# Optimization experiments

Measured on AMD Instinct MI355X. Metric: run time of the kernel, lower is better.

## Reference

```python
import jax, jax.numpy as jnp
import numpy as np

N = 8192
IN_F = 512
OUT_F = 128
NUM_CLASSES = 10
ALPHA = 0.2  # LeakyReLU negative slope
NEG_INF = -9e15


def setup_inputs() -> dict:
    key = jax.random.key(0)
    k_h, k_d, k_W, k_a, k_cw, k_cb = jax.random.split(key, 6)
    h = jax.random.normal(k_h, (N, IN_F), dtype=jnp.float32)
    dist = jax.random.randint(k_d, (N, N), 0, 2, dtype=jnp.int32)
    # xavier_uniform with gain=1.414
    gain = 1.414
    lim_W = gain * np.sqrt(6.0 / (IN_F + OUT_F))
    W = jax.random.uniform(k_W, (IN_F, OUT_F), minval=-lim_W, maxval=lim_W, dtype=jnp.float32)
    lim_a = gain * np.sqrt(6.0 / (2 * OUT_F + 1))
    a = jax.random.uniform(k_a, (2 * OUT_F, 1), minval=-lim_a, maxval=lim_a, dtype=jnp.float32)
    # nn.Linear(out_features, num_classes): weight [C, out], bias [C]
    lim_c = np.sqrt(1.0 / OUT_F)
    Wc = jax.random.uniform(k_cw, (NUM_CLASSES, OUT_F), minval=-lim_c, maxval=lim_c, dtype=jnp.float32)
    bc = jax.random.uniform(k_cb, (NUM_CLASSES,), minval=-lim_c, maxval=lim_c, dtype=jnp.float32)
    return {"h": h, "dist": dist, "W": W, "a": a, "Wc": Wc, "bc": bc}


def reference(h, dist, W, a, Wc, bc):
    Wh = h @ W                              # [N, out]
    Wh1 = Wh @ a[:OUT_F]                    # [N, 1]
    Wh2 = Wh @ a[OUT_F:]                    # [N, 1]
    e = jax.nn.leaky_relu(Wh1 + Wh2.T, negative_slope=ALPHA)  # [N, N]
    att = jnp.where(dist > 0, e, NEG_INF)
    att = jax.nn.softmax(att, axis=1)       # [N, N]
    h_update = jax.nn.elu(att @ Wh)         # [N, out] (dropout inactive at inference)
    y_pred = h_update @ Wc.T + bc           # [N, num_classes]
    return y_pred
```

## Files before the change

### kernel.cpp

```cpp
#include <hip/hip_runtime.h>
#include <stdint.h>

#define N 8192
#define IN_F 512
#define OUT_F 128
#define NCLS 10
#define ALPHA 0.2f

typedef float f32x4 __attribute__((ext_vector_type(4)));
typedef int   i32x4 __attribute__((ext_vector_type(4)));
typedef short s16x4 __attribute__((ext_vector_type(4)));
typedef short s16x8 __attribute__((ext_vector_type(8)));

__device__ __forceinline__ short f2bf(float x) {
    unsigned u = __builtin_bit_cast(unsigned, x);
    u = (u + 0x7FFFu + ((u >> 16) & 1u)) >> 16;
    return (short)u;
}
__device__ __forceinline__ float bf2f(short s) {
    unsigned u = ((unsigned)(unsigned short)s) << 16;
    return __builtin_bit_cast(float, u);
}

__global__ void split_w_kernel(const float* __restrict__ W,
                               short* __restrict__ WThi, short* __restrict__ WTlo) {
    int idx = blockIdx.x * 256 + threadIdx.x;
    int k = idx >> 7, col = idx & 127;
    float x = W[idx];
    short hi = f2bf(x);
    short lo = f2bf(x - bf2f(hi));
    size_t a = (size_t)(k >> 5) * (128 * 32) + (size_t)col * 32 + (k & 31);
    WThi[a] = hi;
    WTlo[a] = lo;
}

#define WH_ROWS 16
#define WH_STR 520

__global__ __launch_bounds__(256, 2)
void wh_kernel(const float* __restrict__ h, const short* __restrict__ WThi,
               const short* __restrict__ WTlo, const float* __restrict__ a,
               short* __restrict__ WhT, float* __restrict__ Wh1,
               float* __restrict__ Wh2) {
    __shared__ __align__(16) short Ahi[WH_ROWS][WH_STR];
    __shared__ __align__(16) short Alo[WH_ROWS][WH_STR];
    __shared__ __align__(16) float whs[WH_ROWS][OUT_F + 4];

    const int t = threadIdx.x;
    const int r0 = blockIdx.x * WH_ROWS;

    {
        int row = t >> 4, c4 = t & 15;
        const float* hrow = h + (size_t)(r0 + row) * IN_F;
        #pragma unroll
        for (int jj = 0; jj < 4; ++jj) {
            int k0 = c4 * 8 + jj * 128;
            f32x4 x0 = *(const f32x4*)(hrow + k0);
            f32x4 x1 = *(const f32x4*)(hrow + k0 + 4);
            s16x8 hi, lo;
            #pragma unroll
            for (int e = 0; e < 4; ++e) {
                short h0 = f2bf(x0[e]); hi[e] = h0; lo[e] = f2bf(x0[e] - bf2f(h0));
                short h1 = f2bf(x1[e]); hi[4 + e] = h1; lo[4 + e] = f2bf(x1[e] - bf2f(h1));
            }
            *(s16x8*)&Ahi[row][k0] = hi;
            *(s16x8*)&Alo[row][k0] = lo;
        }
    }
    __syncthreads();

    const int lane = t & 63, w = t >> 6;
    const int q = lane >> 4, ln16 = lane & 15;
    f32x4 acc[2] = {};
    #pragma unroll
    for (int kc = 0; kc < IN_F / 32; ++kc) {
        s16x8 ahi = *(const s16x8*)&Ahi[ln16][kc * 32 + q * 8];
        s16x8 alo = *(const s16x8*)&Alo[ln16][kc * 32 + q * 8];
        #pragma unroll
        for (int nt = 0; nt < 2; ++nt) {
            int col = w * 32 + nt * 16 + ln16;
            size_t boff = (size_t)kc * 4096 + (size_t)col * 32 + q * 8;
            s16x8 bhi = *(const s16x8*)(WThi + boff);
            s16x8 blo = *(const s16x8*)(WTlo + boff);
            acc[nt] = __builtin_amdgcn_mfma_f32_16x16x32_bf16(ahi, bhi, acc[nt], 0, 0, 0);
            acc[nt] = __builtin_amdgcn_mfma_f32_16x16x32_bf16(ahi, blo, acc[nt], 0, 0, 0);
            acc[nt] = __builtin_amdgcn_mfma_f32_16x16x32_bf16(alo, bhi, acc[nt], 0, 0, 0);
        }
    }
    #pragma unroll
    for (int nt = 0; nt < 2; ++nt)
        #pragma unroll
        for (int reg = 0; reg < 4; ++reg)
            whs[q * 4 + reg][w * 32 + nt * 16 + ln16] = acc[nt][reg];
    __syncthreads();

    if (t < 128) {
        int r = t >> 3, s = t & 7;
        float s1 = 0.f, s2 = 0.f;
        #pragma unroll
        for (int cc = 0; cc < 16; ++cc) {
            int c = s * 16 + cc;
            float v = whs[r][c];
            s1 = fmaf(v, a[c], s1);
            s2 = fmaf(v, a[OUT_F + c], s2);
        }
        s1 += __shfl_xor(s1, 1); s1 += __shfl_xor(s1, 2); s1 += __shfl_xor(s1, 4);
        s2 += __shfl_xor(s2, 1); s2 += __shfl_xor(s2, 2); s2 += __shfl_xor(s2, 4);
        if (s == 0) { Wh1[r0 + r] = s1; Wh2[r0 + r] = s2; }
    }

    {
        int c = t >> 1, h8 = t & 1;
        s16x8 pack;
        #pragma unroll
        for (int rr = 0; rr < 8; ++rr) pack[rr] = f2bf(whs[h8 * 8 + rr][c]);
        size_t addr = (size_t)(r0 >> 5) * 4096 + (size_t)c * 32 + (r0 & 16) + h8 * 8;
        *(s16x8*)(WhT + addr) = pack;
    }
}

#define BK 128

__global__ __launch_bounds__(256, 4)
void attn_kernel(const int* __restrict__ dist, const short* __restrict__ WhT,
                 const float* __restrict__ Wh1v, const float* __restrict__ Wh2v,
                 float* __restrict__ acc_part, float* __restrict__ l_part,
                 int nit) {
    const int t = threadIdx.x;
    const int it = blockIdx.x & 127;
    const int sp = blockIdx.x >> 7;
    const int i0 = it * 64;
    const int lane = t & 63, w = t >> 6;
    const int q = lane >> 4, m = lane & 15;
    const int row = i0 + w * 16 + m;
    const int j0 = sp * nit * BK;

    const int* __restrict__ drow = dist + (size_t)row * N + j0;
    const float* __restrict__ wh2p = Wh2v + j0;
    const float wh1 = Wh1v[row];
    float l_acc = 0.f;
    f32x4 acc[8] = {};

    for (int kt = 0; kt < nit; ++kt) {
        const int jb = kt * BK;
        i32x4 d[8];
        #pragma unroll
        for (int kc = 0; kc < 4; ++kc) {
            d[kc * 2]     = *(const i32x4*)(drow + jb + kc * 32 + q * 8);
            d[kc * 2 + 1] = *(const i32x4*)(drow + jb + kc * 32 + q * 8 + 4);
        }
        s16x8 afr[4];
        #pragma unroll
        for (int kc = 0; kc < 4; ++kc) {
            const float* w2p = wh2p + jb + kc * 32 + q * 8;
            f32x4 w20 = *(const f32x4*)(w2p);
            f32x4 w21 = *(const f32x4*)(w2p + 4);
            #pragma unroll
            for (int e = 0; e < 4; ++e) {
                float sv = wh1 + w20[e];
                float lr = fmaxf(sv, ALPHA * sv);
                float pv = (d[kc * 2][e] > 0) ? __expf(lr) : 0.f;
                l_acc += pv;
                unsigned u = __builtin_bit_cast(unsigned, pv);
                afr[kc][e] = (short)((u + 0x8000u) >> 16);
                float sv1 = wh1 + w21[e];
                float lr1 = fmaxf(sv1, ALPHA * sv1);
                float pv1 = (d[kc * 2 + 1][e] > 0) ? __expf(lr1) : 0.f;
                l_acc += pv1;
                unsigned u1 = __builtin_bit_cast(unsigned, pv1);
                afr[kc][4 + e] = (short)((u1 + 0x8000u) >> 16);
            }
        }
        const short* bb = WhT + (size_t)((j0 + jb) >> 5) * 4096 + q * 8;
        #pragma unroll
        for (int kc = 0; kc < 4; ++kc) {
            const short* bkc = bb + (size_t)kc * 4096;
            #pragma unroll
            for (int nt = 0; nt < 8; ++nt) {
                s16x8 bfr = *(const s16x8*)(bkc + (nt * 16 + m) * 32);
                acc[nt] = __builtin_amdgcn_mfma_f32_16x16x32_bf16(afr[kc], bfr, acc[nt], 0, 0, 0);
            }
        }
    }

    l_acc += __shfl_xor(l_acc, 16);
    l_acc += __shfl_xor(l_acc, 32);
    if (q == 0) l_part[(size_t)sp * N + row] = l_acc;

    float* ap = acc_part + (size_t)sp * N * OUT_F
              + ((size_t)i0 + w * 16 + q * 4) * OUT_F + m;
    #pragma unroll
    for (int reg = 0; reg < 4; ++reg)
        #pragma unroll
        for (int nt = 0; nt < 8; ++nt)
            ap[(size_t)reg * OUT_F + nt * 16] = acc[nt][reg];
}

__global__ __launch_bounds__(256, 4)
void reduce_kernel(const float* __restrict__ acc_part, const float* __restrict__ l_part,
                   const float* __restrict__ Wc, const float* __restrict__ bcv,
                   float* __restrict__ out, int split) {
    __shared__ __align__(16) float hu[16][OUT_F + 4];
    const int t = threadIdx.x;
    const int i0 = blockIdx.x * 16;
    const int row = t >> 4, cg = t & 15;

    f32x4 v0 = {0.f, 0.f, 0.f, 0.f}, v1 = {0.f, 0.f, 0.f, 0.f};
    float l = 0.f;
    for (int s = 0; s < split; ++s) {
        const float* ap = acc_part + (size_t)s * N * OUT_F + (size_t)(i0 + row) * OUT_F + cg * 8;
        v0 += *(const f32x4*)ap;
        v1 += *(const f32x4*)(ap + 4);
        l += l_part[(size_t)s * N + i0 + row];
    }
    float inv = 1.f / l;
    #pragma unroll
    for (int e = 0; e < 4; ++e) {
        float x0 = v0[e] * inv; x0 = x0 > 0.f ? x0 : (__expf(x0) - 1.f);
        float x1 = v1[e] * inv; x1 = x1 > 0.f ? x1 : (__expf(x1) - 1.f);
        hu[row][cg * 8 + e] = x0;
        hu[row][cg * 8 + 4 + e] = x1;
    }
    __syncthreads();

    if (t < 16 * NCLS) {
        int rr = t / NCLS, cls = t - rr * NCLS;
        const f32x4* hurow = (const f32x4*)&hu[rr][0];
        const f32x4* wcrow = (const f32x4*)(Wc + cls * OUT_F);
        float sum = bcv[cls];
        #pragma unroll 8
        for (int c4 = 0; c4 < OUT_F / 4; ++c4) {
            f32x4 hv = hurow[c4];
            f32x4 wv = wcrow[c4];
            sum += hv[0] * wv[0] + hv[1] * wv[1] + hv[2] * wv[2] + hv[3] * wv[3];
        }
        out[(size_t)(i0 + rr) * NCLS + cls] = sum;
    }
}

extern "C" void kernel_launch(void* const* d_in, const int* in_sizes, int n_in,
                              void* d_out, int out_size, void* d_ws, size_t ws_size,
                              hipStream_t stream) {
    const float* h    = (const float*)d_in[0];
    const int*   dist = (const int*)d_in[1];
    const float* W    = (const float*)d_in[2];
    const float* a    = (const float*)d_in[3];
    const float* Wc   = (const float*)d_in[4];
    const float* bc   = (const float*)d_in[5];
    float* out = (float*)d_out;

    char* ws = (char*)d_ws;
    size_t off = 0;
    short* WhT  = (short*)(ws + off); off += (size_t)OUT_F * N * 2;
    short* WThi = (short*)(ws + off); off += (size_t)IN_F * OUT_F * 2;
    short* WTlo = (short*)(ws + off); off += (size_t)IN_F * OUT_F * 2;
    float* Wh1  = (float*)(ws + off); off += (size_t)N * 4;
    float* Wh2  = (float*)(ws + off); off += (size_t)N * 4;

    size_t per_split = (size_t)N * OUT_F * 4 + (size_t)N * 4;
    int split = 8;
    while (split > 1 && off + (size_t)split * per_split > ws_size) split >>= 1;
    float* acc_part = (float*)(ws + off); off += (size_t)split * N * OUT_F * 4;
    float* l_part   = (float*)(ws + off);

    hipLaunchKernelGGL(split_w_kernel, dim3(256), dim3(256), 0, stream, W, WThi, WTlo);
    hipLaunchKernelGGL(wh_kernel, dim3(N / WH_ROWS), dim3(256), 0, stream,
                       h, WThi, WTlo, a, WhT, Wh1, Wh2);
    int nit = N / (BK * split);
    hipLaunchKernelGGL(attn_kernel, dim3(128 * split), dim3(256), 0, stream,
                       dist, WhT, Wh1, Wh2, acc_part, l_part, nit);
    hipLaunchKernelGGL(reduce_kernel, dim3(N / 16), dim3(256), 0, stream,
                       acc_part, l_part, Wc, bc, out, split);
}
```

Measured before the change: 501.6 us.

## Prefetch next dist tile in registers and stagger tile order per block

```diff
diff --git a/kernel.cpp b/kernel.cpp
--- a/kernel.cpp
+++ b/kernel.cpp
@@ -134,6 +134,7 @@
     const int q = lane >> 4, m = lane & 15;
     const int row = i0 + w * 16 + m;
     const int j0 = sp * nit * BK;
+    const int phase = it & (nit - 1);
 
     const int* __restrict__ drow = dist + (size_t)row * N + j0;
     const float* __restrict__ wh2p = Wh2v + j0;
@@ -141,20 +142,50 @@
     float l_acc = 0.f;
     f32x4 acc[8] = {};
 
-    for (int kt = 0; kt < nit; ++kt) {
-        const int jb = kt * BK;
-        i32x4 d[8];
+    i32x4 d[8];
+    f32x4 w2[2][2];
+    {
+        const int jb = phase * BK;
         #pragma unroll
         for (int kc = 0; kc < 4; ++kc) {
             d[kc * 2]     = *(const i32x4*)(drow + jb + kc * 32 + q * 8);
             d[kc * 2 + 1] = *(const i32x4*)(drow + jb + kc * 32 + q * 8 + 4);
         }
+        w2[0][0] = *(const f32x4*)(wh2p + jb + 0 * 32 + q * 8);
+        w2[0][1] = *(const f32x4*)(wh2p + jb + 0 * 32 + q * 8 + 4);
+        w2[1][0] = *(const f32x4*)(wh2p + jb + 1 * 32 + q * 8);
+        w2[1][1] = *(const f32x4*)(wh2p + jb + 1 * 32 + q * 8 + 4);
+    }
+
+    for (int kt = 0; kt < nit; ++kt) {
+        const int cur = (kt + phase) & (nit - 1);
+        const int jb = cur * BK;
+        const bool more = (kt + 1) < nit;
+        const int jbn = (((kt + 1 + phase) & (nit - 1))) * BK;
+
+        i32x4 dn[8];
+        f32x4 w2n[2][2];
+        if (more) {
+            #pragma unroll
+            for (int kc = 0; kc < 4; ++kc) {
+                dn[kc * 2]     = *(const i32x4*)(drow + jbn + kc * 32 + q * 8);
+                dn[kc * 2 + 1] = *(const i32x4*)(drow + jbn + kc * 32 + q * 8 + 4);
+            }
+            w2n[0][0] = *(const f32x4*)(wh2p + jbn + 0 * 32 + q * 8);
+            w2n[0][1] = *(const f32x4*)(wh2p + jbn + 0 * 32 + q * 8 + 4);
+            w2n[1][0] = *(const f32x4*)(wh2p + jbn + 1 * 32 + q * 8);
+            w2n[1][1] = *(const f32x4*)(wh2p + jbn + 1 * 32 + q * 8 + 4);
+        }
+
         s16x8 afr[4];
         #pragma unroll
         for (int kc = 0; kc < 4; ++kc) {
-            const float* w2p = wh2p + jb + kc * 32 + q * 8;
-            f32x4 w20 = *(const f32x4*)(w2p);
-            f32x4 w21 = *(const f32x4*)(w2p + 4);
+            f32x4 w20, w21;
+            if (kc < 2) { w20 = w2[kc][0]; w21 = w2[kc][1]; }
+            else {
+                w20 = *(const f32x4*)(wh2p + jb + kc * 32 + q * 8);
+                w21 = *(const f32x4*)(wh2p + jb + kc * 32 + q * 8 + 4);
+            }
             #pragma unroll
             for (int e = 0; e < 4; ++e) {
                 float sv = wh1 + w20[e];
@@ -181,6 +212,12 @@
                 acc[nt] = __builtin_amdgcn_mfma_f32_16x16x32_bf16(afr[kc], bfr, acc[nt], 0, 0, 0);
             }
         }
+        if (more) {
+            #pragma unroll
+            for (int u = 0; u < 8; ++u) d[u] = dn[u];
+            #pragma unroll
+            for (int u = 0; u < 2; ++u) { w2[u][0] = w2n[u][0]; w2[u][1] = w2n[u][1]; }
+        }
     }
 
     l_acc += __shfl_xor(l_acc, 16);
```

Result: slower. 644.4 us (+28.5%).

## Prefetch dist tile into LDS bitmask with coalesced loads before MFMA loop

Applied to the files above, without the earlier changes.

```diff
diff --git a/kernel.cpp b/kernel.cpp
--- a/kernel.cpp
+++ b/kernel.cpp
@@ -7,9 +7,14 @@
 #define NCLS 10
 #define ALPHA 0.2f
 
+#define WCOLS 1024
+#define NSP (N / WCOLS)
+#define BK 128
+#define NIT (WCOLS / BK)
+#define MSTR 33
+
 typedef float f32x4 __attribute__((ext_vector_type(4)));
 typedef int   i32x4 __attribute__((ext_vector_type(4)));
-typedef short s16x4 __attribute__((ext_vector_type(4)));
 typedef short s16x8 __attribute__((ext_vector_type(8)));
 
 __device__ __forceinline__ short f2bf(float x) {
@@ -119,56 +124,70 @@
     }
 }
 
-#define BK 128
-
 __global__ __launch_bounds__(256, 4)
 void attn_kernel(const int* __restrict__ dist, const short* __restrict__ WhT,
                  const float* __restrict__ Wh1v, const float* __restrict__ Wh2v,
-                 float* __restrict__ acc_part, float* __restrict__ l_part,
-                 int nit) {
+                 float* __restrict__ acc_part, float* __restrict__ l_part) {
+    __shared__ unsigned maskL[64 * MSTR];
+    __shared__ __align__(16) float wh2L[WCOLS];
+
     const int t = threadIdx.x;
     const int it = blockIdx.x & 127;
     const int sp = blockIdx.x >> 7;
     const int i0 = it * 64;
+    const int j0 = sp * WCOLS;
     const int lane = t & 63, w = t >> 6;
     const int q = lane >> 4, m = lane & 15;
+
+    {
+        const int l = lane;
+        #pragma unroll 4
+        for (int rr = 0; rr < 16; ++rr) {
+            const int r = w * 16 + rr;
+            const int* rp = dist + (size_t)(i0 + r) * N + j0 + l * 4;
+            #pragma unroll
+            for (int p = 0; p < 4; ++p) {
+                i32x4 v = *(const i32x4*)(rp + p * 256);
+                unsigned nib = (unsigned)(v[0] > 0) | ((unsigned)(v[1] > 0) << 1)
+                             | ((unsigned)(v[2] > 0) << 2) | ((unsigned)(v[3] > 0) << 3);
+                unsigned b = nib | (__shfl_xor(nib, 1) << 4);
+                b = b | (__shfl_xor(b, 2) << 8);
+                b = b | (__shfl_xor(b, 4) << 16);
+                if ((l & 7) == 0) maskL[r * MSTR + p * 8 + (l >> 3)] = b;
+            }
+        }
+        if (t < WCOLS / 4)
+            *(f32x4*)&wh2L[t * 4] = *(const f32x4*)(Wh2v + j0 + t * 4);
+    }
+    __syncthreads();
+
     const int row = i0 + w * 16 + m;
-    const int j0 = sp * nit * BK;
-
-    const int* __restrict__ drow = dist + (size_t)row * N + j0;
-    const float* __restrict__ wh2p = Wh2v + j0;
     const float wh1 = Wh1v[row];
     float l_acc = 0.f;
     f32x4 acc[8] = {};
-
-    for (int kt = 0; kt < nit; ++kt) {
+    const unsigned* mrow = &maskL[(w * 16 + m) * MSTR];
+
+    for (int kt = 0; kt < NIT; ++kt) {
         const int jb = kt * BK;
-        i32x4 d[8];
+        s16x8 afr[4];
         #pragma unroll
         for (int kc = 0; kc < 4; ++kc) {
-            d[kc * 2]     = *(const i32x4*)(drow + jb + kc * 32 + q * 8);
-            d[kc * 2 + 1] = *(const i32x4*)(drow + jb + kc * 32 + q * 8 + 4);
-        }
-        s16x8 afr[4];
-        #pragma unroll
-        for (int kc = 0; kc < 4; ++kc) {
-            const float* w2p = wh2p + jb + kc * 32 + q * 8;
-            f32x4 w20 = *(const f32x4*)(w2p);
-            f32x4 w21 = *(const f32x4*)(w2p + 4);
+            unsigned mw = mrow[(jb >> 5) + kc];
+            unsigned byq = (mw >> (q * 8)) & 255u;
+            f32x4 w20 = *(const f32x4*)&wh2L[jb + kc * 32 + q * 8];
+            f32x4 w21 = *(const f32x4*)&wh2L[jb + kc * 32 + q * 8 + 4];
             #pragma unroll
             for (int e = 0; e < 4; ++e) {
                 float sv = wh1 + w20[e];
                 float lr = fmaxf(sv, ALPHA * sv);
-                float pv = (d[kc * 2][e] > 0) ? __expf(lr) : 0.f;
+                float pv = ((byq >> e) & 1u) ? __expf(lr) : 0.f;
                 l_acc += pv;
-                unsigned u = __builtin_bit_cast(unsigned, pv);
-                afr[kc][e] = (short)((u + 0x8000u) >> 16);
+                afr[kc][e] = (short)((__builtin_bit_cast(unsigned, pv) + 0x8000u) >> 16);
                 float sv1 = wh1 + w21[e];
                 float lr1 = fmaxf(sv1, ALPHA * sv1);
-                float pv1 = (d[kc * 2 + 1][e] > 0) ? __expf(lr1) : 0.f;
+                float pv1 = ((byq >> (4 + e)) & 1u) ? __expf(lr1) : 0.f;
                 l_acc += pv1;
-                unsigned u1 = __builtin_bit_cast(unsigned, pv1);
-                afr[kc][4 + e] = (short)((u1 + 0x8000u) >> 16);
+                afr[kc][4 + e] = (short)((__builtin_bit_cast(unsigned, pv1) + 0x8000u) >> 16);
             }
         }
         const short* bb = WhT + (size_t)((j0 + jb) >> 5) * 4096 + q * 8;
@@ -199,7 +218,7 @@
 __global__ __launch_bounds__(256, 4)
 void reduce_kernel(const float* __restrict__ acc_part, const float* __restrict__ l_part,
                    const float* __restrict__ Wc, const float* __restrict__ bcv,
-                   float* __restrict__ out, int split) {
+                   float* __restrict__ out) {
     __shared__ __align__(16) float hu[16][OUT_F + 4];
     const int t = threadIdx.x;
     const int i0 = blockIdx.x * 16;
@@ -207,7 +226,7 @@
 
     f32x4 v0 = {0.f, 0.f, 0.f, 0.f}, v1 = {0.f, 0.f, 0.f, 0.f};
     float l = 0.f;
-    for (int s = 0; s < split; ++s) {
+    for (int s = 0; s < NSP; ++s) {
         const float* ap = acc_part + (size_t)s * N * OUT_F + (size_t)(i0 + row) * OUT_F + cg * 8;
         v0 += *(const f32x4*)ap;
         v1 += *(const f32x4*)(ap + 4);
@@ -256,19 +275,14 @@
     short* WTlo = (short*)(ws + off); off += (size_t)IN_F * OUT_F * 2;
     float* Wh1  = (float*)(ws + off); off += (size_t)N * 4;
     float* Wh2  = (float*)(ws + off); off += (size_t)N * 4;
-
-    size_t per_split = (size_t)N * OUT_F * 4 + (size_t)N * 4;
-    int split = 8;
-    while (split > 1 && off + (size_t)split * per_split > ws_size) split >>= 1;
-    float* acc_part = (float*)(ws + off); off += (size_t)split * N * OUT_F * 4;
+    float* acc_part = (float*)(ws + off); off += (size_t)NSP * N * OUT_F * 4;
     float* l_part   = (float*)(ws + off);
 
     hipLaunchKernelGGL(split_w_kernel, dim3(256), dim3(256), 0, stream, W, WThi, WTlo);
     hipLaunchKernelGGL(wh_kernel, dim3(N / WH_ROWS), dim3(256), 0, stream,
                        h, WThi, WTlo, a, WhT, Wh1, Wh2);
-    int nit = N / (BK * split);
-    hipLaunchKernelGGL(attn_kernel, dim3(128 * split), dim3(256), 0, stream,
-                       dist, WhT, Wh1, Wh2, acc_part, l_part, nit);
+    hipLaunchKernelGGL(attn_kernel, dim3(128 * NSP), dim3(256), 0, stream,
+                       dist, WhT, Wh1, Wh2, acc_part, l_part);
     hipLaunchKernelGGL(reduce_kernel, dim3(N / 16), dim3(256), 0, stream,
-                       acc_part, l_part, Wc, bc, out, split);
-}
+                       acc_part, l_part, Wc, bc, out);
+}
```

Measured after the change: 465.2 us. 7.3% less time.
